# Optimization experiments

Measured on AMD Instinct MI355X. Metric: run time of the kernel, lower is better.

The kernel has to match this reference:

```python
import jax, jax.numpy as jnp
import numpy as np

B, W, F = 64, 128, 64          # batch, window (node feat dim), n_features (nodes)
H, OUTW = 4, 128               # num_heads, out window size
NEG_SLOPE = 0.2                # LeakyReLU negative slope (alpha)


def setup_inputs() -> dict:
    key = jax.random.key(0)
    ks = jax.random.split(key, 6)
    scale_in = 1.0 / np.sqrt(W)
    scale_a = 1.0 / np.sqrt(OUTW)
    return {
        "x": jax.random.normal(ks[0], (B, W, F), dtype=jnp.float32),
        "W_src": jax.random.normal(ks[1], (H * OUTW, W), dtype=jnp.float32) * scale_in,
        "b_src": jnp.zeros((H * OUTW,), dtype=jnp.float32),
        "W_dst": jax.random.normal(ks[2], (H * OUTW, W), dtype=jnp.float32) * scale_in,
        "b_dst": jnp.zeros((H * OUTW,), dtype=jnp.float32),
        "attn": jax.random.normal(ks[3], (H, OUTW), dtype=jnp.float32) * scale_a,
    }


def reference(x, W_src, b_src, W_dst, b_dst, attn):
    # x: [B, W, F] -> node features nf: [B, F, W] (F nodes, W-dim features)
    nf = jnp.transpose(x, (0, 2, 1))
    b, f, w = nf.shape
    h, outw = attn.shape
    # GATv2 separate source/destination projections (share_weights=False)
    fs = (nf @ W_src.T + b_src).reshape(b, f, h, outw)  # [B, F, H, outW]
    fd = (nf @ W_dst.T + b_dst).reshape(b, f, h, outw)
    # additive score over complete graph with self-loops: e[b,i,j,h,d]
    s = fs[:, :, None, :, :] + fd[:, None, :, :, :]      # [B, src, dst, H, outW]
    e = jnp.where(s >= 0, s, NEG_SLOPE * s)              # LeakyReLU
    scores = jnp.einsum('bijhd,hd->bhij', e, attn)       # [B, H, src, dst]
    # edge softmax: normalize over incoming edges (sources) per destination
    a = jax.nn.softmax(scores, axis=2)
    # weighted scatter-sum aggregation at destinations
    out = jnp.einsum('bhij,bihd->bjhd', a, fs)           # [B, F, H, outW]
    out = out.mean(axis=2)                               # mean over heads -> [B, F, outW]
    return jnp.transpose(out, (0, 2, 1))                 # [B, outW, F]
```

## Files before the change

kernel.cpp:

```cpp
#include <hip/hip_runtime.h>
#include <math.h>

#define BB 64
#define WW 128
#define FF 64
#define HH 4
#define OW 128


struct GemmRegion {
    float wq[2 * 2 * 128 * 68];
};
struct AttnRegion {
    float fsl[FF * 132];
    float fdl[FF * 132];
    float stT[FF * 68];
    float st2[FF * 68];
    float A6[OW], B4[OW];
    float redm[4 * 64];
    float invl[64];
    float xfer[256 * 36];
};
union SMem { GemmRegion g; AttnRegion a; };

__global__ void __launch_bounds__(512)
__attribute__((amdgpu_waves_per_eu(2, 2)))
gat_fused(
    const float* __restrict__ x,
    const float* __restrict__ Wsrc,
    const float* __restrict__ bsrc,
    const float* __restrict__ Wdst,
    const float* __restrict__ bdst,
    const float* __restrict__ attn,
    float* __restrict__ out)
{
    __shared__ __align__(16) SMem sm;
    __shared__ float bl[2 * 128];

    const int bx = blockIdx.x;
    const int h  = bx & 3;
    const int b  = bx >> 2;
    const int t  = threadIdx.x;

    const int m  = t >> 8;
    const int ig = (t >> 4) & 15;
    const int dg = t & 15;
    const int i0 = ig * 4;

    if (t < 256) bl[t] = (t & 128 ? bdst : bsrc)[h * 128 + (t & 127)];

    const float* xb = x + (size_t)b * (WW * FF);

    #pragma unroll
    for (int p = 0; p < 16; ++p) {
        const int idx = p * 512 + t;
        const int kh = idx >> 12;
        const int mm = (idx >> 11) & 1;
        const int d  = (idx >> 4) & 127;
        const int q  = idx & 15;
        *(float4*)&sm.g.wq[((kh << 8) + mm * 128 + d) * 68 + q * 4] =
            *(const float4*)((mm ? Wdst : Wsrc)
                             + (size_t)(h * 128 + d) * WW + kh * 64 + q * 4);
    }
    __syncthreads();

    float acc[4][8] = {};
    {
        const int wrow = m * 128 + dg;
        #pragma unroll 2
        for (int k0 = 0; k0 < 128; k0 += 4) {
            const int kq = k0 >> 6;
            const int kw = k0 & 63;
            float4 wv[8];
            #pragma unroll
            for (int e = 0; e < 8; ++e)
                wv[e] = *(const float4*)&sm.g.wq[((kq << 8) + wrow + 16 * e) * 68 + kw];
            #pragma unroll
            for (int kk = 0; kk < 4; ++kk) {
                const float4 xv = *(const float4*)(xb + (size_t)(k0 + kk) * FF + i0);
                #pragma unroll
                for (int e = 0; e < 8; ++e) {
                    const float wf = ((const float*)&wv[e])[kk];
                    acc[0][e] = fmaf(xv.x, wf, acc[0][e]);
                    acc[1][e] = fmaf(xv.y, wf, acc[1][e]);
                    acc[2][e] = fmaf(xv.z, wf, acc[2][e]);
                    acc[3][e] = fmaf(xv.w, wf, acc[3][e]);
                }
            }
        }
    }
    __syncthreads();

    {
        float* dst = m ? sm.a.fdl : sm.a.fsl;
        #pragma unroll
        for (int e = 0; e < 8; ++e) {
            const int d = dg + 16 * e;
            const float bv = bl[m * 128 + d];
            #pragma unroll
            for (int ii = 0; ii < 4; ++ii)
                dst[(i0 + ii) * 132 + d] = acc[ii][e] + bv;
        }
    }
    if (t < 128) {
        const float av = attn[h * OW + t];
        sm.a.A6[t] = 0.6f * av;
        sm.a.B4[t] = 0.4f * av;
    }
    __syncthreads();

    if (t < 256) {
        const int i = t & 63, sel = t >> 6;
        const float* src = (sel < 2 ? sm.a.fsl : sm.a.fdl) + i * 132 + (sel & 1) * 64;
        const float* a6  = sm.a.A6 + (sel & 1) * 64;
        float s = 0.0f;
        #pragma unroll
        for (int c = 0; c < 16; ++c) {
            float4 fv = *(const float4*)&src[c * 4];
            float4 av = *(const float4*)&a6[c * 4];
            s = fmaf(fv.x, av.x, fmaf(fv.y, av.y, fmaf(fv.z, av.z, fmaf(fv.w, av.w, s))));
        }
        sm.a.redm[sel * 64 + i] = s;
    }
    __syncthreads();

    {
        const int dh  = t >> 8;
        const int rem = t & 255;
        const int iT  = rem & 15;
        const int j0D = (rem >> 4) * 4;
        float4 scq[4];
        scq[0] = scq[1] = scq[2] = scq[3] = float4{0.f, 0.f, 0.f, 0.f};
        const int cBase = dh * 16;
        #pragma unroll 4
        for (int c = 0; c < 16; ++c) {
            const int dd0 = (cBase + c) * 4;
            const float4 b4 = *(const float4*)&sm.a.B4[dd0];
            float4 fdv[4];
            #pragma unroll
            for (int jj = 0; jj < 4; ++jj)
                fdv[jj] = *(const float4*)&sm.a.fdl[(j0D + jj) * 132 + dd0];
            #pragma unroll
            for (int ii = 0; ii < 4; ++ii) {
                const float4 fsv =
                    *(const float4*)&sm.a.fsl[(iT + 16 * ii) * 132 + dd0];
                float* sc = (float*)&scq[ii];
                #pragma unroll
                for (int jj = 0; jj < 4; ++jj) {
                    float r = sc[jj];
                    r = fmaf(b4.x, fabsf(fsv.x + fdv[jj].x), r);
                    r = fmaf(b4.y, fabsf(fsv.y + fdv[jj].y), r);
                    r = fmaf(b4.z, fabsf(fsv.z + fdv[jj].z), r);
                    r = fmaf(b4.w, fabsf(fsv.w + fdv[jj].w), r);
                    sc[jj] = r;
                }
            }
        }
        if (dh) {
            #pragma unroll
            for (int ii = 0; ii < 4; ++ii)
                *(float4*)&sm.a.st2[(iT + 16 * ii) * 68 + j0D] = scq[ii];
        }
        __syncthreads();
        if (!dh) {
            float cdj[4];
            #pragma unroll
            for (int jj = 0; jj < 4; ++jj)
                cdj[jj] = sm.a.redm[128 + j0D + jj] + sm.a.redm[192 + j0D + jj];
            #pragma unroll
            for (int ii = 0; ii < 4; ++ii) {
                const int i = iT + 16 * ii;
                const float4 p2 = *(const float4*)&sm.a.st2[i * 68 + j0D];
                const float csl = sm.a.redm[i] + sm.a.redm[64 + i];
                const float* sc = (const float*)&scq[ii];
                const float* pp = (const float*)&p2;
                #pragma unroll
                for (int jj = 0; jj < 4; ++jj)
                    sm.a.stT[(j0D + jj) * 68 + i] = sc[jj] + pp[jj] + csl + cdj[jj];
            }
        }
    }
    __syncthreads();

    {
        const int j   = t >> 3;
        const int sub = t & 7;
        float* rp = &sm.a.stT[j * 68 + sub * 8];
        float4 r0 = *(const float4*)(rp);
        float4 r1 = *(const float4*)(rp + 4);
        float mx = fmaxf(fmaxf(fmaxf(r0.x, r0.y), fmaxf(r0.z, r0.w)),
                         fmaxf(fmaxf(r1.x, r1.y), fmaxf(r1.z, r1.w)));
        #pragma unroll
        for (int o = 1; o < 8; o <<= 1) mx = fmaxf(mx, __shfl_xor(mx, o));
        float4 e0, e1;
        e0.x = __expf(r0.x - mx); e0.y = __expf(r0.y - mx);
        e0.z = __expf(r0.z - mx); e0.w = __expf(r0.w - mx);
        e1.x = __expf(r1.x - mx); e1.y = __expf(r1.y - mx);
        e1.z = __expf(r1.z - mx); e1.w = __expf(r1.w - mx);
        float s = e0.x + e0.y + e0.z + e0.w + e1.x + e1.y + e1.z + e1.w;
        #pragma unroll
        for (int o = 1; o < 8; o <<= 1) s += __shfl_xor(s, o);
        *(float4*)(rp)     = e0;
        *(float4*)(rp + 4) = e1;
        if (sub == 0) sm.a.invl[j] = 0.25f / s;
    }
    __syncthreads();

    {
        const int ih  = t >> 8;
        const int rem = t & 255;
        const int jT  = rem & 15;
        const int dgF = rem >> 4;
        const int dF  = dgF * 4;
        const int iBase = ih * 32;

        float ag[4][8] = {};
        #pragma unroll 2
        for (int i2 = 0; i2 < 32; i2 += 4) {
            float4 pq[4];
            #pragma unroll
            for (int jj = 0; jj < 4; ++jj)
                pq[jj] = *(const float4*)&sm.a.stT[(jT + 16 * jj) * 68 + iBase + i2];
            #pragma unroll
            for (int u = 0; u < 4; ++u) {
                const int i = iBase + i2 + u;
                const float4 f0 = *(const float4*)&sm.a.fsl[i * 132 + dF];
                const float4 f1 = *(const float4*)&sm.a.fsl[i * 132 + dF + 64];
                #pragma unroll
                for (int jj = 0; jj < 4; ++jj) {
                    const float p = ((const float*)&pq[jj])[u];
                    ag[jj][0] = fmaf(p, f0.x, ag[jj][0]);
                    ag[jj][1] = fmaf(p, f0.y, ag[jj][1]);
                    ag[jj][2] = fmaf(p, f0.z, ag[jj][2]);
                    ag[jj][3] = fmaf(p, f0.w, ag[jj][3]);
                    ag[jj][4] = fmaf(p, f1.x, ag[jj][4]);
                    ag[jj][5] = fmaf(p, f1.y, ag[jj][5]);
                    ag[jj][6] = fmaf(p, f1.z, ag[jj][6]);
                    ag[jj][7] = fmaf(p, f1.w, ag[jj][7]);
                }
            }
        }

        if (ih) {
            #pragma unroll
            for (int jj = 0; jj < 4; ++jj) {
                float4 a0 = {ag[jj][0], ag[jj][1], ag[jj][2], ag[jj][3]};
                float4 a1 = {ag[jj][4], ag[jj][5], ag[jj][6], ag[jj][7]};
                *(float4*)&sm.a.xfer[rem * 36 + jj * 8]     = a0;
                *(float4*)&sm.a.xfer[rem * 36 + jj * 8 + 4] = a1;
            }
        }
        __syncthreads();
        if (!ih) {
            float* ob = out + (size_t)b * OW * FF;
            #pragma unroll
            for (int jj = 0; jj < 4; ++jj) {
                const float4 a0 = *(const float4*)&sm.a.xfer[rem * 36 + jj * 8];
                const float4 a1 = *(const float4*)&sm.a.xfer[rem * 36 + jj * 8 + 4];
                const float iv = sm.a.invl[jT + 16 * jj];
                const int j = jT + 16 * jj;
                atomicAdd(ob + (size_t)(dF + 0) * FF + j, (ag[jj][0] + a0.x) * iv);
                atomicAdd(ob + (size_t)(dF + 1) * FF + j, (ag[jj][1] + a0.y) * iv);
                atomicAdd(ob + (size_t)(dF + 2) * FF + j, (ag[jj][2] + a0.z) * iv);
                atomicAdd(ob + (size_t)(dF + 3) * FF + j, (ag[jj][3] + a0.w) * iv);
                atomicAdd(ob + (size_t)(dF + 64) * FF + j, (ag[jj][4] + a1.x) * iv);
                atomicAdd(ob + (size_t)(dF + 65) * FF + j, (ag[jj][5] + a1.y) * iv);
                atomicAdd(ob + (size_t)(dF + 66) * FF + j, (ag[jj][6] + a1.z) * iv);
                atomicAdd(ob + (size_t)(dF + 67) * FF + j, (ag[jj][7] + a1.w) * iv);
            }
        }
    }
}

extern "C" void kernel_launch(void* const* d_in, const int* in_sizes, int n_in,
                              void* d_out, int out_size, void* d_ws, size_t ws_size,
                              hipStream_t stream) {
    const float* x    = (const float*)d_in[0];
    const float* Wsrc = (const float*)d_in[1];
    const float* bsrc = (const float*)d_in[2];
    const float* Wdst = (const float*)d_in[3];
    const float* bdst = (const float*)d_in[4];
    const float* attn = (const float*)d_in[5];

    hipMemsetAsync(d_out, 0, (size_t)out_size, stream);
    gat_fused<<<BB * HH, 512, 0, stream>>>(x, Wsrc, bsrc, Wdst, bdst, attn,
                                           (float*)d_out);
}
```

Before: 100.4 us.

## Double block to 1024 threads with split-K projection GEMM and LDS reduction

The block grows from 512 to 1024 threads. The projection GEMM is split along K between two thread halves, and the partial sums are combined through a new shared-memory exchange region. The later attention stages keep 512 active threads, so the extra threads sit idle there while still taking part in the barriers. The aim is more parallelism and latency hiding in the GEMM phase. The cost is an extra LDS exchange with extra barriers, a dropped waves_per_eu hint, and higher register pressure per block, which may lower occupancy.

```diff
diff --git a/kernel.cpp b/kernel.cpp
--- a/kernel.cpp
+++ b/kernel.cpp
@@ -21,10 +21,13 @@
     float invl[64];
     float xfer[256 * 36];
 };
-union SMem { GemmRegion g; AttnRegion a; };
-
-__global__ void __launch_bounds__(512)
-__attribute__((amdgpu_waves_per_eu(2, 2)))
+struct ExRegion {
+    float pad[FF * 132 * 2];
+    float ex[512 * 36];
+};
+union SMem { GemmRegion g; AttnRegion a; ExRegion e; };
+
+__global__ void __launch_bounds__(1024)
 gat_fused(
     const float* __restrict__ x,
     const float* __restrict__ Wsrc,
@@ -42,42 +45,43 @@
     const int b  = bx >> 2;
     const int t  = threadIdx.x;
 
-    const int m  = t >> 8;
-    const int ig = (t >> 4) & 15;
-    const int dg = t & 15;
-    const int i0 = ig * 4;
+    const int kh   = t >> 9;
+    const int rem9 = t & 511;
+    const int m    = rem9 >> 8;
+    const int ig   = (rem9 >> 4) & 15;
+    const int dg   = rem9 & 15;
+    const int i0   = ig * 4;
 
     if (t < 256) bl[t] = (t & 128 ? bdst : bsrc)[h * 128 + (t & 127)];
 
     const float* xb = x + (size_t)b * (WW * FF);
 
     #pragma unroll
-    for (int p = 0; p < 16; ++p) {
-        const int idx = p * 512 + t;
-        const int kh = idx >> 12;
+    for (int p = 0; p < 8; ++p) {
+        const int idx = p * 1024 + t;
+        const int k2 = idx >> 12;
         const int mm = (idx >> 11) & 1;
         const int d  = (idx >> 4) & 127;
         const int q  = idx & 15;
-        *(float4*)&sm.g.wq[((kh << 8) + mm * 128 + d) * 68 + q * 4] =
+        *(float4*)&sm.g.wq[((k2 << 8) + mm * 128 + d) * 68 + q * 4] =
             *(const float4*)((mm ? Wdst : Wsrc)
-                             + (size_t)(h * 128 + d) * WW + kh * 64 + q * 4);
+                             + (size_t)(h * 128 + d) * WW + k2 * 64 + q * 4);
     }
     __syncthreads();
 
     float acc[4][8] = {};
     {
-        const int wrow = m * 128 + dg;
+        const int wbase = (kh << 8) + m * 128 + dg;
+        const float* xk = xb + (size_t)(kh * 64) * FF;
         #pragma unroll 2
-        for (int k0 = 0; k0 < 128; k0 += 4) {
-            const int kq = k0 >> 6;
-            const int kw = k0 & 63;
+        for (int k0 = 0; k0 < 64; k0 += 4) {
             float4 wv[8];
             #pragma unroll
             for (int e = 0; e < 8; ++e)
-                wv[e] = *(const float4*)&sm.g.wq[((kq << 8) + wrow + 16 * e) * 68 + kw];
+                wv[e] = *(const float4*)&sm.g.wq[(wbase + 16 * e) * 68 + k0];
             #pragma unroll
             for (int kk = 0; kk < 4; ++kk) {
-                const float4 xv = *(const float4*)(xb + (size_t)(k0 + kk) * FF + i0);
+                const float4 xv = *(const float4*)(xk + (size_t)(k0 + kk) * FF + i0);
                 #pragma unroll
                 for (int e = 0; e < 8; ++e) {
                     const float wf = ((const float*)&wv[e])[kk];
@@ -91,17 +95,35 @@
     }
     __syncthreads();
 
-    {
+    if (kh) {
+        #pragma unroll
+        for (int ii = 0; ii < 4; ++ii) {
+            float4 a0 = {acc[ii][0], acc[ii][1], acc[ii][2], acc[ii][3]};
+            float4 a1 = {acc[ii][4], acc[ii][5], acc[ii][6], acc[ii][7]};
+            *(float4*)&sm.e.ex[rem9 * 36 + ii * 8]     = a0;
+            *(float4*)&sm.e.ex[rem9 * 36 + ii * 8 + 4] = a1;
+        }
+    }
+    __syncthreads();
+
+    if (!kh) {
         float* dst = m ? sm.a.fdl : sm.a.fsl;
         #pragma unroll
-        for (int e = 0; e < 8; ++e) {
-            const int d = dg + 16 * e;
-            const float bv = bl[m * 128 + d];
-            #pragma unroll
-            for (int ii = 0; ii < 4; ++ii)
-                dst[(i0 + ii) * 132 + d] = acc[ii][e] + bv;
-        }
-    }
+        for (int ii = 0; ii < 4; ++ii) {
+            const float4 p0 = *(const float4*)&sm.e.ex[rem9 * 36 + ii * 8];
+            const float4 p1 = *(const float4*)&sm.e.ex[rem9 * 36 + ii * 8 + 4];
+            const float* pp0 = (const float*)&p0;
+            const float* pp1 = (const float*)&p1;
+            #pragma unroll
+            for (int e = 0; e < 8; ++e) {
+                const int d = dg + 16 * e;
+                const float pv = (e < 4) ? pp0[e] : pp1[e - 4];
+                dst[(i0 + ii) * 132 + d] = acc[ii][e] + pv + bl[m * 128 + d];
+            }
+        }
+    }
+    __syncthreads();
+
     if (t < 128) {
         const float av = attn[h * OW + t];
         sm.a.A6[t] = 0.6f * av;
@@ -125,44 +147,47 @@
     __syncthreads();
 
     {
-        const int dh  = t >> 8;
+        const bool act = t < 512;
+        const int dh  = (t >> 8) & 1;
         const int rem = t & 255;
         const int iT  = rem & 15;
         const int j0D = (rem >> 4) * 4;
         float4 scq[4];
         scq[0] = scq[1] = scq[2] = scq[3] = float4{0.f, 0.f, 0.f, 0.f};
-        const int cBase = dh * 16;
-        #pragma unroll 4
-        for (int c = 0; c < 16; ++c) {
-            const int dd0 = (cBase + c) * 4;
-            const float4 b4 = *(const float4*)&sm.a.B4[dd0];
-            float4 fdv[4];
-            #pragma unroll
-            for (int jj = 0; jj < 4; ++jj)
-                fdv[jj] = *(const float4*)&sm.a.fdl[(j0D + jj) * 132 + dd0];
-            #pragma unroll
-            for (int ii = 0; ii < 4; ++ii) {
-                const float4 fsv =
-                    *(const float4*)&sm.a.fsl[(iT + 16 * ii) * 132 + dd0];
-                float* sc = (float*)&scq[ii];
-                #pragma unroll
-                for (int jj = 0; jj < 4; ++jj) {
-                    float r = sc[jj];
-                    r = fmaf(b4.x, fabsf(fsv.x + fdv[jj].x), r);
-                    r = fmaf(b4.y, fabsf(fsv.y + fdv[jj].y), r);
-                    r = fmaf(b4.z, fabsf(fsv.z + fdv[jj].z), r);
-                    r = fmaf(b4.w, fabsf(fsv.w + fdv[jj].w), r);
-                    sc[jj] = r;
+        if (act) {
+            const int cBase = dh * 16;
+            #pragma unroll 4
+            for (int c = 0; c < 16; ++c) {
+                const int dd0 = (cBase + c) * 4;
+                const float4 b4 = *(const float4*)&sm.a.B4[dd0];
+                float4 fdv[4];
+                #pragma unroll
+                for (int jj = 0; jj < 4; ++jj)
+                    fdv[jj] = *(const float4*)&sm.a.fdl[(j0D + jj) * 132 + dd0];
+                #pragma unroll
+                for (int ii = 0; ii < 4; ++ii) {
+                    const float4 fsv =
+                        *(const float4*)&sm.a.fsl[(iT + 16 * ii) * 132 + dd0];
+                    float* sc = (float*)&scq[ii];
+                    #pragma unroll
+                    for (int jj = 0; jj < 4; ++jj) {
+                        float r = sc[jj];
+                        r = fmaf(b4.x, fabsf(fsv.x + fdv[jj].x), r);
+                        r = fmaf(b4.y, fabsf(fsv.y + fdv[jj].y), r);
+                        r = fmaf(b4.z, fabsf(fsv.z + fdv[jj].z), r);
+                        r = fmaf(b4.w, fabsf(fsv.w + fdv[jj].w), r);
+                        sc[jj] = r;
+                    }
                 }
             }
-        }
-        if (dh) {
-            #pragma unroll
-            for (int ii = 0; ii < 4; ++ii)
-                *(float4*)&sm.a.st2[(iT + 16 * ii) * 68 + j0D] = scq[ii];
+            if (dh) {
+                #pragma unroll
+                for (int ii = 0; ii < 4; ++ii)
+                    *(float4*)&sm.a.st2[(iT + 16 * ii) * 68 + j0D] = scq[ii];
+            }
         }
         __syncthreads();
-        if (!dh) {
+        if (act && !dh) {
             float cdj[4];
             #pragma unroll
             for (int jj = 0; jj < 4; ++jj)
@@ -182,7 +207,7 @@
     }
     __syncthreads();
 
-    {
+    if (t < 512) {
         const int j   = t >> 3;
         const int sub = t & 7;
         float* rp = &sm.a.stT[j * 68 + sub * 8];
@@ -207,7 +232,8 @@
     __syncthreads();
 
     {
-        const int ih  = t >> 8;
+        const bool act = t < 512;
+        const int ih  = (t >> 8) & 1;
         const int rem = t & 255;
         const int jT  = rem & 15;
         const int dgF = rem >> 4;
@@ -215,43 +241,44 @@
         const int iBase = ih * 32;
 
         float ag[4][8] = {};
-        #pragma unroll 2
-        for (int i2 = 0; i2 < 32; i2 += 4) {
-            float4 pq[4];
-            #pragma unroll
-            for (int jj = 0; jj < 4; ++jj)
-                pq[jj] = *(const float4*)&sm.a.stT[(jT + 16 * jj) * 68 + iBase + i2];
-            #pragma unroll
-            for (int u = 0; u < 4; ++u) {
-                const int i = iBase + i2 + u;
-                const float4 f0 = *(const float4*)&sm.a.fsl[i * 132 + dF];
-                const float4 f1 = *(const float4*)&sm.a.fsl[i * 132 + dF + 64];
+        if (act) {
+            #pragma unroll 2
+            for (int i2 = 0; i2 < 32; i2 += 4) {
+                float4 pq[4];
+                #pragma unroll
+                for (int jj = 0; jj < 4; ++jj)
+                    pq[jj] = *(const float4*)&sm.a.stT[(jT + 16 * jj) * 68 + iBase + i2];
+                #pragma unroll
+                for (int u = 0; u < 4; ++u) {
+                    const int i = iBase + i2 + u;
+                    const float4 f0 = *(const float4*)&sm.a.fsl[i * 132 + dF];
+                    const float4 f1 = *(const float4*)&sm.a.fsl[i * 132 + dF + 64];
+                    #pragma unroll
+                    for (int jj = 0; jj < 4; ++jj) {
+                        const float p = ((const float*)&pq[jj])[u];
+                        ag[jj][0] = fmaf(p, f0.x, ag[jj][0]);
+                        ag[jj][1] = fmaf(p, f0.y, ag[jj][1]);
+                        ag[jj][2] = fmaf(p, f0.z, ag[jj][2]);
+                        ag[jj][3] = fmaf(p, f0.w, ag[jj][3]);
+                        ag[jj][4] = fmaf(p, f1.x, ag[jj][4]);
+                        ag[jj][5] = fmaf(p, f1.y, ag[jj][5]);
+                        ag[jj][6] = fmaf(p, f1.z, ag[jj][6]);
+                        ag[jj][7] = fmaf(p, f1.w, ag[jj][7]);
+                    }
+                }
+            }
+            if (ih) {
                 #pragma unroll
                 for (int jj = 0; jj < 4; ++jj) {
-                    const float p = ((const float*)&pq[jj])[u];
-                    ag[jj][0] = fmaf(p, f0.x, ag[jj][0]);
-                    ag[jj][1] = fmaf(p, f0.y, ag[jj][1]);
-                    ag[jj][2] = fmaf(p, f0.z, ag[jj][2]);
-                    ag[jj][3] = fmaf(p, f0.w, ag[jj][3]);
-                    ag[jj][4] = fmaf(p, f1.x, ag[jj][4]);
-                    ag[jj][5] = fmaf(p, f1.y, ag[jj][5]);
-                    ag[jj][6] = fmaf(p, f1.z, ag[jj][6]);
-                    ag[jj][7] = fmaf(p, f1.w, ag[jj][7]);
+                    float4 a0 = {ag[jj][0], ag[jj][1], ag[jj][2], ag[jj][3]};
+                    float4 a1 = {ag[jj][4], ag[jj][5], ag[jj][6], ag[jj][7]};
+                    *(float4*)&sm.a.xfer[rem * 36 + jj * 8]     = a0;
+                    *(float4*)&sm.a.xfer[rem * 36 + jj * 8 + 4] = a1;
                 }
             }
         }
-
-        if (ih) {
-            #pragma unroll
-            for (int jj = 0; jj < 4; ++jj) {
-                float4 a0 = {ag[jj][0], ag[jj][1], ag[jj][2], ag[jj][3]};
-                float4 a1 = {ag[jj][4], ag[jj][5], ag[jj][6], ag[jj][7]};
-                *(float4*)&sm.a.xfer[rem * 36 + jj * 8]     = a0;
-                *(float4*)&sm.a.xfer[rem * 36 + jj * 8 + 4] = a1;
-            }
-        }
         __syncthreads();
-        if (!ih) {
+        if (act && !ih) {
             float* ob = out + (size_t)b * OW * FF;
             #pragma unroll
             for (int jj = 0; jj < 4; ++jj) {
@@ -283,6 +310,6 @@
     const float* attn = (const float*)d_in[5];
 
     hipMemsetAsync(d_out, 0, (size_t)out_size, stream);
-    gat_fused<<<BB * HH, 512, 0, stream>>>(x, Wsrc, bsrc, Wdst, bdst, attn,
-                                           (float*)d_out);
+    gat_fused<<<BB * HH, 1024, 0, stream>>>(x, Wsrc, bsrc, Wdst, bdst, attn,
+                                            (float*)d_out);
 }
```

New measurement: 105.2 us. +4.8%, slower.
